# Performance work log

Measured on AMD Instinct MI355X. Metric: run time of the kernel, lower is better.

Reference implementation:

```python
import jax, jax.numpy as jnp
import numpy as np

N = 4096          # num nodes
D = 128           # feature dim (dataset.x.shape[-1])
E = 131072        # num edges (avg degree 32)
POOL_K = 0.6      # ks[0]
K = max(2, int(POOL_K * N))  # 2457 kept nodes


def setup_inputs() -> dict:
    key = jax.random.key(0)
    ks = jax.random.split(key, 8)
    s = 0.05
    g = jax.random.randint(ks[0], (2, E), 0, N)                      # edge_index
    h = jax.random.normal(ks[1], (N, D), jnp.float32)                # node features
    Wd = jax.random.normal(ks[2], (D, D), jnp.float32) * s           # down-GCN stub
    bd = jnp.zeros((D,), jnp.float32)
    pw = jax.random.normal(ks[3], (D, 1), jnp.float32) * s           # Pool.proj weight
    pb = jnp.zeros((1,), jnp.float32)                                # Pool.proj bias
    Wb = jax.random.normal(ks[4], (D, D), jnp.float32) * s           # bottom-GCN stub
    bb = jnp.zeros((D,), jnp.float32)
    Wu = jax.random.normal(ks[5], (D, D), jnp.float32) * s           # up-GCN stub
    bu = jnp.zeros((D,), jnp.float32)
    return {"g": g, "h": h, "Wd": Wd, "bd": bd, "pw": pw, "pb": pb,
            "Wb": Wb, "bb": bb, "Wu": Wu, "bu": bu}


def reference(g, h, Wd, bd, pw, pb, Wb, bb, Wu, bu):
    dt = h.dtype
    src, dst = g[0], g[1]
    # to_dense_adj: scatter-add edges into dense [N, N] adjacency
    adj = jnp.zeros((N, N), dt).at[src, dst].add(jnp.ones((E,), dt))

    # down GCN (GNNEarly stub, called with h only): linear
    h0 = h @ Wd + bd

    # Pool: score, topk, gather
    scores = jax.nn.sigmoid((h0 @ pw + pb)[:, 0])          # [N]
    values, idx = jax.lax.top_k(scores, K)                 # descending, like torch.topk
    new_h = h0[idx] * values[:, None]                      # [K, D]

    # boolean 2-hop connectivity, then subselect pooled nodes
    un_g = (adj > 0).astype(dt)
    two_hop = ((un_g @ un_g) > 0).astype(dt)               # [N, N]
    sub = two_hop[idx][:, idx]                             # [K, K]
    # norm_g: g / degrees with torch broadcasting => column-normalize by row-degree
    degrees = jnp.sum(sub, axis=1)                         # [K]
    g_p = sub / degrees                                    # sub[i,j] / degrees[j]

    # bottom GCN (stub with pooled graph): propagate + linear
    h_b = g_p @ (new_h @ Wb) + bb                          # [K, D]

    # Unpool: scatter back to N nodes
    h_u = jnp.zeros((N, D), dt).at[idx].set(h_b)

    # up GCN (stub with original dense adj adj_ms[0])
    h_up = adj @ (h_u @ Wu) + bu                           # [N, D]

    h1 = h_up + h0        # h.add(down_outs[0])
    h2 = h1 + h           # h.add(org_h)
    return (h1, h2)       # hs list
```

## Files before the change

### kernel.cpp

```cpp
#include <hip/hip_runtime.h>
#include <hip/hip_bf16.h>
#include <stdint.h>


#define NN 4096
#define DD 128
#define KKEEP 2457
#define SUBW 40
#define MP 2464
#define KP 2560
#define MT 154
#define NT 8
#define KCHUNK (KP / 4)
#define RT 8

typedef unsigned long long u64;
typedef unsigned short ushort_t;
typedef __attribute__((ext_vector_type(8))) short bf16x8;
typedef __attribute__((ext_vector_type(4))) float f32x4;

__global__ void k_zero(float4* __restrict__ p) {
    int i = blockIdx.x * 256 + threadIdx.x;
    p[i] = make_float4(0.f, 0.f, 0.f, 0.f);
}

__global__ void k_h0_build(const float* __restrict__ h, const float* __restrict__ Wd,
                           const float* __restrict__ bd, const float* __restrict__ pw,
                           const float* __restrict__ pb, const int* __restrict__ g, int E,
                           const float* __restrict__ Wb, const float* __restrict__ Wu,
                           const float* __restrict__ bb,
                           float* __restrict__ h0, float* __restrict__ scores,
                           u64* __restrict__ rowbits, int* __restrict__ deg,
                           float* __restrict__ W2, float* __restrict__ cu) {
    __shared__ float rows[RT][DD];
    __shared__ float sred[2][RT];
    int bid = blockIdx.x;
    int d = threadIdx.x;
    if (bid >= 1536) {
        int wb = bid - 1536;
        if (wb < 16) {
            int r0 = wb * RT;
            #pragma unroll
            for (int r = 0; r < RT; ++r) rows[r][d] = Wb[(size_t)(r0 + r) * DD + d];
            __syncthreads();
            float acc[RT];
            #pragma unroll
            for (int r = 0; r < RT; ++r) acc[r] = 0.f;
            for (int kb = 0; kb < DD; kb += 16) {
                float w[16];
                #pragma unroll
                for (int j = 0; j < 16; ++j) w[j] = Wu[(size_t)(kb + j) * DD + d];
                #pragma unroll
                for (int r = 0; r < RT; ++r)
                    #pragma unroll
                    for (int j = 0; j < 16; ++j) acc[r] += rows[r][kb + j] * w[j];
            }
            #pragma unroll
            for (int r = 0; r < RT; ++r) W2[(size_t)(r0 + r) * DD + d] = acc[r];
        } else {
            float a = 0.f;
            for (int m = 0; m < DD; ++m) a += bb[m] * Wu[(size_t)m * DD + d];
            cu[d] = a;
        }
        return;
    }
    if (bid >= 512) {
        int e = (bid - 512) * 128 + d;
        if (e < E) {
            int s = g[e], d2 = g[E + e];
            atomicOr(&rowbits[(size_t)s * 64 + (d2 >> 6)], 1ull << (d2 & 63));
            atomicAdd(&deg[s], 1);
        }
        return;
    }
    int r0 = bid * RT;
    #pragma unroll
    for (int r = 0; r < RT; ++r) rows[r][d] = h[(size_t)(r0 + r) * DD + d];
    __syncthreads();
    float acc[RT];
    float b = bd[d];
    #pragma unroll
    for (int r = 0; r < RT; ++r) acc[r] = b;
    for (int kb = 0; kb < DD; kb += 16) {
        float w[16];
        #pragma unroll
        for (int j = 0; j < 16; ++j) w[j] = Wd[(size_t)(kb + j) * DD + d];
        #pragma unroll
        for (int r = 0; r < RT; ++r)
            #pragma unroll
            for (int j = 0; j < 16; ++j) acc[r] += rows[r][kb + j] * w[j];
    }
    #pragma unroll
    for (int r = 0; r < RT; ++r) h0[(size_t)(r0 + r) * DD + d] = acc[r];
    float pwd = pw[d];
    int lane = d & 63, wv = d >> 6;
    #pragma unroll
    for (int r = 0; r < RT; ++r) {
        float v = acc[r] * pwd;
        #pragma unroll
        for (int s = 32; s > 0; s >>= 1) v += __shfl_xor(v, s);
        if (lane == 0) sred[wv][r] = v;
    }
    __syncthreads();
    if (d < RT) {
        float v = sred[0][d] + sred[1][d];
        scores[r0 + d] = 1.0f / (1.0f + expf(-(v + pb[0])));
    }
}

__global__ void k_rank_scan(const float* __restrict__ scores, const int* __restrict__ deg,
                            int* __restrict__ keep, int* __restrict__ pos,
                            int* __restrict__ idxl, int* __restrict__ off) {
    int bid = blockIdx.x;
    int t = threadIdx.x;
    if (bid == NN / 4) {
        __shared__ int part[256];
        int base = t * 16;
        int loc[16]; int s = 0;
        #pragma unroll
        for (int i = 0; i < 16; ++i) { loc[i] = s; s += deg[base + i]; }
        part[t] = s;
        __syncthreads();
        int sum = 0;
        for (int i = 0; i < t; ++i) sum += part[i];
        #pragma unroll
        for (int i = 0; i < 16; ++i) off[base + i] = sum + loc[i];
        if (t == 255) off[NN] = sum + s;
        return;
    }
    int lane = t & 63;
    int i = bid * 4 + (t >> 6);
    float my = scores[i];
    int rank = 0;
    #pragma unroll 4
    for (int base = 0; base < NN; base += 64) {
        int jj = base + lane;
        float sj = scores[jj];
        u64 m = __ballot((sj > my) || (sj == my && jj < i));
        rank += __popcll(m);
    }
    if (lane == 0) {
        if (rank < KKEEP) { keep[i] = 1; pos[i] = rank; idxl[rank] = i; }
        else keep[i] = 0;
    }
}

__global__ void k_sub_scatter(const u64* __restrict__ rowbits, const int* __restrict__ idxl,
                              const int* __restrict__ g, int E, const int* __restrict__ off,
                              const int* __restrict__ keep, const int* __restrict__ pos,
                              int* __restrict__ cursor, int* __restrict__ csrv,
                              u64* __restrict__ subbits, float* __restrict__ invdeg) {
    __shared__ int nb[320];
    __shared__ int nbcnt;
    __shared__ int cntS;
    __shared__ u64 accLDS[64];
    int bid = blockIdx.x;
    int t = threadIdx.x;
    if (bid >= MP) {
        int e = (bid - MP) * 256 + t;
        if (e < E) {
            int s = g[e], dd = g[E + e];
            int p = atomicAdd(&cursor[s], 1);
            csrv[off[s] + p] = keep[dd] ? pos[dd] : -1;
        }
        return;
    }
    int r = bid;
    int wv = t >> 6, lane = t & 63;
    if (r >= KKEEP) {
        if (t < SUBW) subbits[(size_t)r * SUBW + t] = 0;
        return;
    }
    int i = idxl[r];
    if (wv == 0) {
        u64 rw = rowbits[(size_t)i * 64 + lane];
        int myc = __popcll(rw);
        int pre = myc;
        #pragma unroll
        for (int s2 = 1; s2 < 64; s2 <<= 1) {
            int tt = __shfl_up(pre, s2);
            if (lane >= s2) pre += tt;
        }
        pre -= myc;
        u64 w = rw; int j = 0;
        while (w) {
            int b = __builtin_ctzll(w);
            w &= w - 1;
            nb[pre + j] = lane * 64 + b; ++j;
        }
        if (lane == 63) nbcnt = pre + myc;
    } else if (wv == 1) {
        accLDS[lane] = 0;
    } else if (wv == 2 && lane == 0) {
        cntS = 0;
    }
    __syncthreads();
    int cnt_nb = nbcnt;
    u64 accw = 0;
    for (int j = wv; j < cnt_nb; j += 4)
        accw |= rowbits[(size_t)nb[j] * 64 + lane];
    atomicOr(&accLDS[lane], accw);
    __syncthreads();
    u64 accw_full = accLDS[lane];
    int cntp = 0;
    #pragma unroll
    for (int wjj = 0; wjj < 10; ++wjj) {
        int wj = wv * 10 + wjj;
        int c = wj * 64 + lane;
        int ci = (c < KKEEP) ? idxl[c] : 0;
        u64 w = __shfl(accw_full, ci >> 6);
        int bit = (c < KKEEP) ? (int)((w >> (ci & 63)) & 1ull) : 0;
        u64 word = __ballot(bit);
        cntp += __popcll(word);
        if (lane == 0) subbits[(size_t)r * SUBW + wj] = word;
    }
    if (lane == 0) atomicAdd(&cntS, cntp);
    __syncthreads();
    if (t == 0) invdeg[r] = 1.0f / (float)cntS;
}

__global__ void k_t(const float* __restrict__ h0, const float* __restrict__ scores,
                    const int* __restrict__ idxl, const float* __restrict__ W2,
                    const float* __restrict__ invdeg, ushort_t* __restrict__ tT) {
    __shared__ float rows[RT][DD];
    int d = threadIdx.x;
    int r0 = blockIdx.x * RT;
    #pragma unroll
    for (int r = 0; r < RT; ++r) {
        int rr = r0 + r;
        float v = 0.f;
        if (rr < KKEEP) {
            int i = idxl[rr];
            v = h0[(size_t)i * DD + d] * scores[i];
        }
        rows[r][d] = v;
    }
    __syncthreads();
    float acc[RT];
    #pragma unroll
    for (int r = 0; r < RT; ++r) acc[r] = 0.f;
    for (int kb = 0; kb < DD; kb += 16) {
        float w[16];
        #pragma unroll
        for (int j = 0; j < 16; ++j) w[j] = W2[(size_t)(kb + j) * DD + d];
        #pragma unroll
        for (int r = 0; r < RT; ++r)
            #pragma unroll
            for (int j = 0; j < 16; ++j) acc[r] += rows[r][kb + j] * w[j];
    }
    bf16x8 packed;
    #pragma unroll
    for (int r = 0; r < RT; ++r) {
        int rr = r0 + r;
        float v = (rr < KKEEP) ? acc[r] * invdeg[rr] : 0.f;
        __hip_bfloat16 b = __float2bfloat16(v);
        packed[r] = *reinterpret_cast<short*>(&b);
    }
    *reinterpret_cast<bf16x8*>(tT + (size_t)d * KP + r0) = packed;
}

__global__ void k_gemm(const u64* __restrict__ subbits, const short* __restrict__ tT,
                       const float* __restrict__ cu, float* __restrict__ uu) {
    __shared__ f32x4 red[4][64];
    __shared__ uint4 lut[256];
    int t = threadIdx.x;
    {
        uint32_t x0 = ((t & 1) ? 0x3F80u : 0u) | ((t & 2) ? 0x3F800000u : 0u);
        uint32_t x1 = ((t & 4) ? 0x3F80u : 0u) | ((t & 8) ? 0x3F800000u : 0u);
        uint32_t x2 = ((t & 16) ? 0x3F80u : 0u) | ((t & 32) ? 0x3F800000u : 0u);
        uint32_t x3 = ((t & 64) ? 0x3F80u : 0u) | ((t & 128) ? 0x3F800000u : 0u);
        lut[t] = make_uint4(x0, x1, x2, x3);
    }
    __syncthreads();
    int bid = blockIdx.x;
    int tile = (bid & 7) * (MT * NT / 8) + (bid >> 3);
    int wv = t >> 6, lane = t & 63;
    int rt = tile >> 3, ct = tile & 7;
    const u64* abits = subbits + (size_t)(rt * 16 + (lane & 15)) * SUBW;
    const short* brow = tT + (size_t)(ct * 16 + (lane & 15)) * KP + ((lane >> 4) * 8) + wv * KCHUNK;
    int kbase = wv * KCHUNK + ((lane >> 4) * 8);
    f32x4 acc = {0.f, 0.f, 0.f, 0.f};
    #pragma unroll 4
    for (int kk = 0; kk < KCHUNK; kk += 32) {
        int k = kbase + kk;
        u64 w = abits[k >> 6];
        int byte = (int)((w >> (k & 63)) & 0xFFull);
        uint4 af = lut[byte];
        bf16x8 a = *reinterpret_cast<bf16x8*>(&af);
        bf16x8 b = *(const bf16x8*)(brow + kk);
        acc = __builtin_amdgcn_mfma_f32_16x16x32_bf16(a, b, acc, 0, 0, 0);
    }
    red[wv][lane] = acc;
    __syncthreads();
    if (wv == 0) {
        f32x4 s = red[0][lane] + red[1][lane] + red[2][lane] + red[3][lane];
        int col = ct * 16 + (lane & 15);
        float cuv = cu[col];
        int row0 = rt * 16 + ((lane >> 4) * 4);
        #pragma unroll
        for (int j = 0; j < 4; ++j) {
            int row = row0 + j;
            if (row < KKEEP) uu[(size_t)row * DD + col] = s[j] + cuv;
        }
    }
}

__global__ void k_agg(const int* __restrict__ off, const int* __restrict__ csrv,
                      const float* __restrict__ uu, const float* __restrict__ bu,
                      const float* __restrict__ h0, const float* __restrict__ h,
                      float* __restrict__ out) {
    int s = blockIdx.x, d = threadIdx.x;
    int b = off[s], e2 = off[s + 1];
    float acc = 0.f;
    int k = b;
    for (; k + 4 <= e2; k += 4) {
        int v0 = csrv[k], v1 = csrv[k + 1], v2 = csrv[k + 2], v3 = csrv[k + 3];
        float a0 = (v0 >= 0) ? uu[(size_t)v0 * DD + d] : 0.f;
        float a1 = (v1 >= 0) ? uu[(size_t)v1 * DD + d] : 0.f;
        float a2 = (v2 >= 0) ? uu[(size_t)v2 * DD + d] : 0.f;
        float a3 = (v3 >= 0) ? uu[(size_t)v3 * DD + d] : 0.f;
        acc += (a0 + a1) + (a2 + a3);
    }
    for (; k < e2; ++k) {
        int v = csrv[k];
        if (v >= 0) acc += uu[(size_t)v * DD + d];
    }
    size_t o = (size_t)s * DD + d;
    float a = acc + bu[d] + h0[o];
    out[o] = a;
    out[(size_t)NN * DD + o] = a + h[o];
}

extern "C" void kernel_launch(void* const* d_in, const int* in_sizes, int n_in,
                              void* d_out, int out_size, void* d_ws, size_t ws_size,
                              hipStream_t stream) {
    const int*   g  = (const int*)d_in[0];
    const float* h  = (const float*)d_in[1];
    const float* Wd = (const float*)d_in[2];
    const float* bd = (const float*)d_in[3];
    const float* pw = (const float*)d_in[4];
    const float* pb = (const float*)d_in[5];
    const float* Wb = (const float*)d_in[6];
    const float* bb = (const float*)d_in[7];
    const float* Wu = (const float*)d_in[8];
    const float* bu = (const float*)d_in[9];
    float* out = (float*)d_out;
    int E = in_sizes[0] / 2;

    char* ws = (char*)d_ws;
    u64*      subbits = (u64*)  (ws + 0);
    u64*      rowbits = (u64*)  (ws + (13u << 20));
    int*      deg     = (int*)  (ws + (15u << 20));
    int*      cursor  = (int*)  (ws + (15u << 20) + 16384);
    int*      off     = (int*)  (ws + (15u << 20) + 32768);
    float*    h0      = (float*)(ws + (16u << 20));
    ushort_t* tT      = (ushort_t*)(ws + (18u << 20));
    int*      csrv    = (int*)  (ws + (21u << 20));
    float*    uu      = (float*)(ws + (22u << 20));
    float*    scores  = (float*)(ws + (24u << 20));
    float*    invdeg  = (float*)(ws + (24u << 20) + 16384);
    int*      pos     = (int*)  (ws + (24u << 20) + 32768);
    int*      keep    = (int*)  (ws + (24u << 20) + 49152);
    int*      idxl    = (int*)  (ws + (24u << 20) + 65536);
    float*    W2      = (float*)(ws + (24u << 20) + 98304);
    float*    cu      = (float*)(ws + (24u << 20) + 98304 + 65536);

    k_zero<<<520, 256, 0, stream>>>((float4*)rowbits);
    k_h0_build<<<1553, 128, 0, stream>>>(h, Wd, bd, pw, pb, g, E, Wb, Wu, bb,
                                         h0, scores, rowbits, deg, W2, cu);
    k_rank_scan<<<NN / 4 + 1, 256, 0, stream>>>(scores, deg, keep, pos, idxl, off);
    k_sub_scatter<<<MP + E / 256, 256, 0, stream>>>(rowbits, idxl, g, E, off,
                                                    keep, pos, cursor, csrv, subbits, invdeg);
    k_t<<<KP / RT, DD, 0, stream>>>(h0, scores, idxl, W2, invdeg, tT);
    k_gemm<<<MT * NT, 256, 0, stream>>>(subbits, (const short*)tT, cu, uu);
    k_agg<<<NN, DD, 0, stream>>>(off, csrv, uu, bu, h0, h, out);
}
```

Baseline: 107.8 us.

## Fuse pooled-feature transform into sub-scatter kernel; apply inverse degree inside GEMM

The separate k_t launch is removed, and its work (gathering pooled rows, multiplying by W2, writing bf16 transposed tT) now runs as extra blocks of the sub-scatter kernel. This breaks the dependency on invdeg, which k_t previously applied per row. Instead, the GEMM's bit-to-bf16 LUT now produces masks that are ANDed with a bf16 invdeg vector, so the column normalization happens while the A operand is expanded. This saves one kernel launch and lets the transform overlap with the scatter work. The cost is an extra invdeg load per MFMA step and invdeg rounded to bf16. The invdeg read at k up to KP-1 for padded rows may touch uninitialized memory, but those products are masked to zero.

```diff
diff --git a/kernel.cpp b/kernel.cpp
--- a/kernel.cpp
+++ b/kernel.cpp
@@ -13,6 +13,7 @@
 #define NT 8
 #define KCHUNK (KP / 4)
 #define RT 8
+#define TBLK 160
 
 typedef unsigned long long u64;
 typedef unsigned short ushort_t;
@@ -145,17 +146,57 @@
     }
 }
 
-__global__ void k_sub_scatter(const u64* __restrict__ rowbits, const int* __restrict__ idxl,
-                              const int* __restrict__ g, int E, const int* __restrict__ off,
-                              const int* __restrict__ keep, const int* __restrict__ pos,
-                              int* __restrict__ cursor, int* __restrict__ csrv,
-                              u64* __restrict__ subbits, float* __restrict__ invdeg) {
+__global__ void k_sub_scatter_t(const u64* __restrict__ rowbits, const int* __restrict__ idxl,
+                                const int* __restrict__ g, int E, const int* __restrict__ off,
+                                const int* __restrict__ keep, const int* __restrict__ pos,
+                                int* __restrict__ cursor, int* __restrict__ csrv,
+                                u64* __restrict__ subbits, ushort_t* __restrict__ invdegb,
+                                const float* __restrict__ h0, const float* __restrict__ scores,
+                                const float* __restrict__ W2, ushort_t* __restrict__ tT) {
+    __shared__ float rowsLDS[16][DD];
     __shared__ int nb[320];
     __shared__ int nbcnt;
     __shared__ int cntS;
     __shared__ u64 accLDS[64];
     int bid = blockIdx.x;
     int t = threadIdx.x;
+    if (bid >= MP + 512) {
+        int u = bid - (MP + 512);
+        int half = t >> 7, d = t & 127;
+        int r0 = u * 16 + half * 8;
+        float (*rows)[DD] = &rowsLDS[half * 8];
+        #pragma unroll
+        for (int r = 0; r < RT; ++r) {
+            int rr = r0 + r;
+            float v = 0.f;
+            if (rr < KKEEP) {
+                int i = idxl[rr];
+                v = h0[(size_t)i * DD + d] * scores[i];
+            }
+            rows[r][d] = v;
+        }
+        __syncthreads();
+        float acc[RT];
+        #pragma unroll
+        for (int r = 0; r < RT; ++r) acc[r] = 0.f;
+        for (int kb = 0; kb < DD; kb += 16) {
+            float w[16];
+            #pragma unroll
+            for (int j = 0; j < 16; ++j) w[j] = W2[(size_t)(kb + j) * DD + d];
+            #pragma unroll
+            for (int r = 0; r < RT; ++r)
+                #pragma unroll
+                for (int j = 0; j < 16; ++j) acc[r] += rows[r][kb + j] * w[j];
+        }
+        bf16x8 packed;
+        #pragma unroll
+        for (int r = 0; r < RT; ++r) {
+            __hip_bfloat16 b = __float2bfloat16(acc[r]);
+            packed[r] = *reinterpret_cast<short*>(&b);
+        }
+        *reinterpret_cast<bf16x8*>(tT + (size_t)d * KP + r0) = packed;
+        return;
+    }
     if (bid >= MP) {
         int e = (bid - MP) * 256 + t;
         if (e < E) {
@@ -216,60 +257,24 @@
     }
     if (lane == 0) atomicAdd(&cntS, cntp);
     __syncthreads();
-    if (t == 0) invdeg[r] = 1.0f / (float)cntS;
-}
-
-__global__ void k_t(const float* __restrict__ h0, const float* __restrict__ scores,
-                    const int* __restrict__ idxl, const float* __restrict__ W2,
-                    const float* __restrict__ invdeg, ushort_t* __restrict__ tT) {
-    __shared__ float rows[RT][DD];
-    int d = threadIdx.x;
-    int r0 = blockIdx.x * RT;
-    #pragma unroll
-    for (int r = 0; r < RT; ++r) {
-        int rr = r0 + r;
-        float v = 0.f;
-        if (rr < KKEEP) {
-            int i = idxl[rr];
-            v = h0[(size_t)i * DD + d] * scores[i];
-        }
-        rows[r][d] = v;
-    }
-    __syncthreads();
-    float acc[RT];
-    #pragma unroll
-    for (int r = 0; r < RT; ++r) acc[r] = 0.f;
-    for (int kb = 0; kb < DD; kb += 16) {
-        float w[16];
-        #pragma unroll
-        for (int j = 0; j < 16; ++j) w[j] = W2[(size_t)(kb + j) * DD + d];
-        #pragma unroll
-        for (int r = 0; r < RT; ++r)
-            #pragma unroll
-            for (int j = 0; j < 16; ++j) acc[r] += rows[r][kb + j] * w[j];
-    }
-    bf16x8 packed;
-    #pragma unroll
-    for (int r = 0; r < RT; ++r) {
-        int rr = r0 + r;
-        float v = (rr < KKEEP) ? acc[r] * invdeg[rr] : 0.f;
-        __hip_bfloat16 b = __float2bfloat16(v);
-        packed[r] = *reinterpret_cast<short*>(&b);
-    }
-    *reinterpret_cast<bf16x8*>(tT + (size_t)d * KP + r0) = packed;
-}
-
-__global__ void k_gemm(const u64* __restrict__ subbits, const short* __restrict__ tT,
-                       const float* __restrict__ cu, float* __restrict__ uu) {
+    if (t == 0) {
+        __hip_bfloat16 b = __float2bfloat16(1.0f / (float)cntS);
+        invdegb[r] = *reinterpret_cast<ushort_t*>(&b);
+    }
+}
+
+__global__ void k_gemm(const u64* __restrict__ subbits, const ushort_t* __restrict__ invdegb,
+                       const short* __restrict__ tT, const float* __restrict__ cu,
+                       float* __restrict__ uu) {
     __shared__ f32x4 red[4][64];
     __shared__ uint4 lut[256];
     int t = threadIdx.x;
     {
-        uint32_t x0 = ((t & 1) ? 0x3F80u : 0u) | ((t & 2) ? 0x3F800000u : 0u);
-        uint32_t x1 = ((t & 4) ? 0x3F80u : 0u) | ((t & 8) ? 0x3F800000u : 0u);
-        uint32_t x2 = ((t & 16) ? 0x3F80u : 0u) | ((t & 32) ? 0x3F800000u : 0u);
-        uint32_t x3 = ((t & 64) ? 0x3F80u : 0u) | ((t & 128) ? 0x3F800000u : 0u);
-        lut[t] = make_uint4(x0, x1, x2, x3);
+        uint32_t m0 = ((t & 1) ? 0xFFFFu : 0u) | ((t & 2) ? 0xFFFF0000u : 0u);
+        uint32_t m1 = ((t & 4) ? 0xFFFFu : 0u) | ((t & 8) ? 0xFFFF0000u : 0u);
+        uint32_t m2 = ((t & 16) ? 0xFFFFu : 0u) | ((t & 32) ? 0xFFFF0000u : 0u);
+        uint32_t m3 = ((t & 64) ? 0xFFFFu : 0u) | ((t & 128) ? 0xFFFF0000u : 0u);
+        lut[t] = make_uint4(m0, m1, m2, m3);
     }
     __syncthreads();
     int bid = blockIdx.x;
@@ -285,7 +290,9 @@
         int k = kbase + kk;
         u64 w = abits[k >> 6];
         int byte = (int)((w >> (k & 63)) & 0xFFull);
-        uint4 af = lut[byte];
+        uint4 msk = lut[byte];
+        uint4 ivb = *(const uint4*)(invdegb + k);
+        uint4 af = make_uint4(msk.x & ivb.x, msk.y & ivb.y, msk.z & ivb.z, msk.w & ivb.w);
         bf16x8 a = *reinterpret_cast<bf16x8*>(&af);
         bf16x8 b = *(const bf16x8*)(brow + kk);
         acc = __builtin_amdgcn_mfma_f32_16x16x32_bf16(a, b, acc, 0, 0, 0);
@@ -358,7 +365,7 @@
     int*      csrv    = (int*)  (ws + (21u << 20));
     float*    uu      = (float*)(ws + (22u << 20));
     float*    scores  = (float*)(ws + (24u << 20));
-    float*    invdeg  = (float*)(ws + (24u << 20) + 16384);
+    ushort_t* invdegb = (ushort_t*)(ws + (24u << 20) + 16384);
     int*      pos     = (int*)  (ws + (24u << 20) + 32768);
     int*      keep    = (int*)  (ws + (24u << 20) + 49152);
     int*      idxl    = (int*)  (ws + (24u << 20) + 65536);
@@ -369,9 +376,9 @@
     k_h0_build<<<1553, 128, 0, stream>>>(h, Wd, bd, pw, pb, g, E, Wb, Wu, bb,
                                          h0, scores, rowbits, deg, W2, cu);
     k_rank_scan<<<NN / 4 + 1, 256, 0, stream>>>(scores, deg, keep, pos, idxl, off);
-    k_sub_scatter<<<MP + E / 256, 256, 0, stream>>>(rowbits, idxl, g, E, off,
-                                                    keep, pos, cursor, csrv, subbits, invdeg);
-    k_t<<<KP / RT, DD, 0, stream>>>(h0, scores, idxl, W2, invdeg, tT);
-    k_gemm<<<MT * NT, 256, 0, stream>>>(subbits, (const short*)tT, cu, uu);
+    k_sub_scatter_t<<<MP + 512 + TBLK, 256, 0, stream>>>(rowbits, idxl, g, E, off,
+                                                         keep, pos, cursor, csrv,
+                                                         subbits, invdegb, h0, scores, W2, tT);
+    k_gemm<<<MT * NT, 256, 0, stream>>>(subbits, invdegb, (const short*)tT, cu, uu);
     k_agg<<<NN, DD, 0, stream>>>(off, csrv, uu, bu, h0, h, out);
 }
```

New measurement: 110.2 us. 2.2% more time.
